# Kernel optimization log

Measured on AMD Instinct MI355X. Metric: run time of the kernel, lower is better.

The kernel has to match this reference:

```python
import jax, jax.numpy as jnp
import numpy as np

DIM = 128
HEADS = 8
HD = DIM // HEADS          # head_dim = 16
KD = HD // 2               # key_dim = 8 (attn_ratio=0.5)
EPS = 1e-3                 # BatchNorm eps
SCALE = KD ** -0.5


def _bn(x, g, b, m, v):
    # eval-mode BatchNorm2d over channel axis (NCHW)
    s = (g / jnp.sqrt(v + EPS))[None, :, None, None]
    return (x - m[None, :, None, None]) * s + b[None, :, None, None]


def _conv1x1(x, w):
    # w: [Cout, Cin, 1, 1]
    return jnp.einsum('oi,bihw->bohw', w[:, :, 0, 0], x)


def _dwconv3(x, w):
    # depthwise 3x3, pad 1; w: [C, 1, 3, 3]
    return jax.lax.conv_general_dilated(
        x, w, window_strides=(1, 1), padding=((1, 1), (1, 1)),
        feature_group_count=x.shape[1],
        dimension_numbers=('NCHW', 'OIHW', 'NCHW'))


def setup_inputs() -> dict:
    key = jax.random.key(0)
    ks = jax.random.split(key, 20)
    H_CH = DIM + 2 * KD * HEADS  # 256
    x = jax.random.normal(ks[0], (4, DIM, 40, 40), dtype=jnp.float32)

    def bn_params(k, c):
        k1, k2, k3, k4 = jax.random.split(k, 4)
        g = 1.0 + 0.1 * jax.random.normal(k1, (c,), jnp.float32)
        b = 0.1 * jax.random.normal(k2, (c,), jnp.float32)
        m = 0.1 * jax.random.normal(k3, (c,), jnp.float32)
        v = jax.random.uniform(k4, (c,), jnp.float32, 0.5, 1.5)
        return g, b, m, v

    qkv_w = 0.05 * jax.random.normal(ks[1], (H_CH, DIM, 1, 1), jnp.float32)
    qkv_g, qkv_b, qkv_m, qkv_v = bn_params(ks[2], H_CH)
    pe_w = 0.05 * jax.random.normal(ks[3], (DIM, 1, 3, 3), jnp.float32)
    pe_g, pe_b, pe_m, pe_v = bn_params(ks[4], DIM)
    proj_w = 0.05 * jax.random.normal(ks[5], (DIM, DIM, 1, 1), jnp.float32)
    proj_g, proj_b, proj_m, proj_v = bn_params(ks[6], DIM)

    return dict(x=x,
                qkv_w=qkv_w, qkv_g=qkv_g, qkv_b=qkv_b, qkv_m=qkv_m, qkv_v=qkv_v,
                pe_w=pe_w, pe_g=pe_g, pe_b=pe_b, pe_m=pe_m, pe_v=pe_v,
                proj_w=proj_w, proj_g=proj_g, proj_b=proj_b, proj_m=proj_m, proj_v=proj_v)


def reference(x, qkv_w, qkv_g, qkv_b, qkv_m, qkv_v,
              pe_w, pe_g, pe_b, pe_m, pe_v,
              proj_w, proj_g, proj_b, proj_m, proj_v):
    b, c, H, W = x.shape
    n = H * W
    qkv = _bn(_conv1x1(x, qkv_w), qkv_g, qkv_b, qkv_m, qkv_v)
    qkv = qkv.reshape(b, HEADS, 2 * KD + HD, n)
    q, k, v = qkv[:, :, :KD], qkv[:, :, KD:2 * KD], qkv[:, :, 2 * KD:]
    # attn[b,h,n,m] = sum_k q[b,h,k,n] * k[b,h,k,m] * scale
    attn = jnp.einsum('bhkn,bhkm->bhnm', q, k) * SCALE
    attn = jax.nn.softmax(attn, axis=-1)
    # out = v @ attn^T : [b,h,hd,n]
    out = jnp.einsum('bhdn,bhmn->bhdm', v, attn).reshape(b, c, H, W)
    pe = _bn(_dwconv3(v.reshape(b, c, H, W), pe_w), pe_g, pe_b, pe_m, pe_v)
    y = _bn(_conv1x1(out + pe, proj_w), proj_g, proj_b, proj_m, proj_v)
    return y
```

## Files before the change

kernel.cpp:

```cpp
#include <hip/hip_runtime.h>
#include <hip/hip_bf16.h>

#define NB 4
#define CDIM 128
#define NPIX 1600
#define WIMG 40
#define HCH 256
#define NHEADS 8
#define KDQ 8
#define HDV 16
#define EPSV 1e-3f
#define SCALEV 0.35355339059327373f
#define KT 320
#define KLP 24
#define VTP (KT + 8)

typedef unsigned short u16;
typedef float f32x4 __attribute__((ext_vector_type(4)));
typedef __bf16 bf16x8 __attribute__((ext_vector_type(8)));

union U16B { uint4 u; bf16x8 v; };

__device__ __forceinline__ u16 f2bf(float f) {
  unsigned u = __float_as_uint(f);
  return (u16)((u + 0x7FFFu + ((u >> 16) & 1u)) >> 16);
}
__device__ __forceinline__ float bf2f(u16 b) {
  return __uint_as_float(((unsigned)b) << 16);
}
__device__ __forceinline__ unsigned cvt_pk_bf16(float lo, float hi) {
  unsigned r;
  asm("v_cvt_pk_bf16_f32 %0, %1, %2" : "=v"(r) : "v"(lo), "v"(hi));
  return r;
}

__global__ __launch_bounds__(512) void k_qkv(
    const float* __restrict__ x, const float* __restrict__ w,
    const float* __restrict__ gg, const float* __restrict__ bb,
    const float* __restrict__ mm, const float* __restrict__ vv,
    float* __restrict__ vf32, u16* __restrict__ qbf,
    u16* __restrict__ kbf, u16* __restrict__ vtbf)
{
  const int pblk = blockIdx.x % 7;
  const int ct   = (blockIdx.x / 7) % (HCH / 8);
  const int b    = blockIdx.x / (7 * (HCH / 8));
  const int tid  = threadIdx.x;
  const int half = tid >> 8;
  const int t    = tid & 255;

  __shared__ float wl[8][CDIM];
  __shared__ float red[256][8];
  for (int i = tid; i < 8 * CDIM; i += 512)
    wl[i >> 7][i & 127] = w[(ct * 8 + (i >> 7)) * CDIM + (i & 127)];
  __syncthreads();

  const int praw = pblk * 256 + t;
  const int p    = praw < NPIX ? praw : NPIX - 1;

  const float* xb = x + (size_t)b * CDIM * NPIX + p;
  float acc[8] = {0.f, 0.f, 0.f, 0.f, 0.f, 0.f, 0.f, 0.f};
  const int c0 = half * 64;
#pragma unroll 4
  for (int ci = c0; ci < c0 + 64; ++ci) {
    const float xv = xb[(size_t)ci * NPIX];
#pragma unroll
    for (int j = 0; j < 8; ++j) acc[j] += wl[j][ci] * xv;
  }

  if (half == 1) {
#pragma unroll
    for (int j = 0; j < 8; ++j) red[t][j] = acc[j];
  }
  __syncthreads();
  if (half == 1 || praw >= NPIX) return;
#pragma unroll
  for (int j = 0; j < 8; ++j) acc[j] += red[t][j];

  const int grp = ct & 3;
  const int h   = ct >> 2;
  float o[8];
#pragma unroll
  for (int j = 0; j < 8; ++j) {
    const int c = ct * 8 + j;
    const float sc = gg[c] * rsqrtf(vv[c] + EPSV);
    const float bi = bb[c] - mm[c] * sc;
    o[j] = acc[j] * sc + bi;
    if (grp == 0) o[j] *= SCALEV;
  }

  if (grp <= 1) {
    u16 hb[8], lb[8];
#pragma unroll
    for (int j = 0; j < 8; ++j) {
      hb[j] = f2bf(o[j]);
      lb[j] = f2bf(o[j] - bf2f(hb[j]));
    }
    uint4 H, L;
    H.x = hb[0] | ((unsigned)hb[1] << 16);
    H.y = hb[2] | ((unsigned)hb[3] << 16);
    H.z = hb[4] | ((unsigned)hb[5] << 16);
    H.w = hb[6] | ((unsigned)hb[7] << 16);
    L.x = lb[0] | ((unsigned)lb[1] << 16);
    L.y = lb[2] | ((unsigned)lb[3] << 16);
    L.z = lb[4] | ((unsigned)lb[5] << 16);
    L.w = lb[6] | ((unsigned)lb[7] << 16);
    u16* dst = (grp == 0) ? qbf : kbf;
    const size_t base = ((size_t)(b * NHEADS + h) * NPIX + p) * 16;
    *(uint4*)&dst[base]     = H;
    *(uint4*)&dst[base + 8] = L;
  } else {
    const int d0 = (grp == 2) ? 0 : 8;
#pragma unroll
    for (int j = 0; j < 8; ++j) {
      vtbf[((size_t)(b * NHEADS + h) * HDV + d0 + j) * NPIX + p] = f2bf(o[j]);
      vf32[((size_t)b * CDIM + h * HDV + d0 + j) * NPIX + p] = o[j];
    }
  }
}

__global__ __launch_bounds__(256) void k_peadd(
    const float* __restrict__ vf32, const float* __restrict__ w,
    const float* __restrict__ gg, const float* __restrict__ bb,
    const float* __restrict__ mm, const float* __restrict__ vv,
    float* __restrict__ atb)
{
  const int idx = blockIdx.x * 256 + threadIdx.x;
  if (idx >= NB * CDIM * NPIX) return;
  const int p  = idx % NPIX;
  const int vc = (idx / NPIX) % CDIM;
  const int yy = p / WIMG, xx = p % WIMG;
  const float* vb = vf32 + (size_t)(idx - p);
  float acc = 0.f;
#pragma unroll
  for (int dy = -1; dy <= 1; ++dy)
#pragma unroll
    for (int dx = -1; dx <= 1; ++dx) {
      const int y2 = yy + dy, x2 = xx + dx;
      if ((unsigned)y2 < (unsigned)WIMG && (unsigned)x2 < (unsigned)WIMG)
        acc += w[vc * 9 + (dy + 1) * 3 + (dx + 1)] * vb[y2 * WIMG + x2];
    }
  const float sc = gg[vc] * rsqrtf(vv[vc] + EPSV);
  const float bi = bb[vc] - mm[vc] * sc;
  atb[idx] += acc * sc + bi;
}

__global__ __launch_bounds__(256) void k_attn(
    const u16* __restrict__ qbf, const u16* __restrict__ kbf,
    const u16* __restrict__ vtbf, float* __restrict__ attno)
{
  const int bh   = blockIdx.x & 31;
  const int qblk = blockIdx.x >> 5;
  const int b = bh >> 3, h = bh & 7;
  const int tid = threadIdx.x;
  const int lane = tid & 63, wid = tid >> 6;
  const int qloc = lane & 15, g = lane >> 4;

  __shared__ __align__(16) u16 Klds[KT][KLP];
  __shared__ __align__(16) u16 Vtlds[HDV][VTP];

  const int qglob = qblk * 64 + wid * 16 + qloc;
  U16B qf;
  qf.u = *(const uint4*)&qbf[((size_t)bh * NPIX + qglob) * 16 + (g & 1) * 8];

  f32x4 c3 = {0.f, 0.f, 0.f, 0.f};
  float lsum = 0.f;
  const int idx0 = (((g & 1) << 5) | qloc) << 2;
  const int idx1 = idx0 + 64;
  const bool selA = (g < 2);
  const f32x4 zf = {0.f, 0.f, 0.f, 0.f};
  const int ksel = (g >> 1) * 8;

  for (int kt = 0; kt < NPIX / KT; ++kt) {
    const int kb0 = kt * KT;
    __syncthreads();
    for (int i = tid; i < KT * 2; i += 256) {
      const int r = i >> 1, hf = (i & 1) * 8;
      *(uint4*)&Klds[r][hf] =
          *(const uint4*)&kbf[((size_t)bh * NPIX + kb0 + r) * 16 + hf];
    }
    for (int c = tid; c < HDV * (KT / 8); c += 256) {
      const int d = c / (KT / 8), n0 = (c % (KT / 8)) * 8;
      *(uint4*)&Vtlds[d][n0] =
          *(const uint4*)&vtbf[((size_t)bh * HDV + d) * NPIX + kb0 + n0];
    }
    __syncthreads();

    for (int ks = 0; ks < KT / 32; ++ks) {
      U16B kfA, kfB;
      kfA.u = *(const uint4*)&Klds[ks * 32 + qloc][ksel];
      kfB.u = *(const uint4*)&Klds[ks * 32 + 16 + qloc][ksel];
      f32x4 cA = __builtin_amdgcn_mfma_f32_16x16x32_bf16(kfA.v, qf.v, zf, 0, 0, 0);
      f32x4 cB = __builtin_amdgcn_mfma_f32_16x16x32_bf16(kfB.v, qf.v, zf, 0, 0, 0);

      const unsigned pkA0 = cvt_pk_bf16(__expf(cA[0]), __expf(cA[1]));
      const unsigned pkA1 = cvt_pk_bf16(__expf(cA[2]), __expf(cA[3]));
      const unsigned pkB0 = cvt_pk_bf16(__expf(cB[0]), __expf(cB[1]));
      const unsigned pkB1 = cvt_pk_bf16(__expf(cB[2]), __expf(cB[3]));

      const int a0 = __builtin_amdgcn_ds_bpermute(idx0, (int)pkA0);
      const int b0 = __builtin_amdgcn_ds_bpermute(idx0, (int)pkB0);
      const int a1 = __builtin_amdgcn_ds_bpermute(idx0, (int)pkA1);
      const int b1 = __builtin_amdgcn_ds_bpermute(idx0, (int)pkB1);
      const int a2 = __builtin_amdgcn_ds_bpermute(idx1, (int)pkA0);
      const int b2 = __builtin_amdgcn_ds_bpermute(idx1, (int)pkB0);
      const int a3 = __builtin_amdgcn_ds_bpermute(idx1, (int)pkA1);
      const int b3 = __builtin_amdgcn_ds_bpermute(idx1, (int)pkB1);
      U16B pf;
      pf.u.x = (unsigned)(selA ? a0 : b0);
      pf.u.y = (unsigned)(selA ? a1 : b1);
      pf.u.z = (unsigned)(selA ? a2 : b2);
      pf.u.w = (unsigned)(selA ? a3 : b3);

      lsum += __uint_as_float(pf.u.x << 16) + __uint_as_float(pf.u.x & 0xFFFF0000u)
            + __uint_as_float(pf.u.y << 16) + __uint_as_float(pf.u.y & 0xFFFF0000u)
            + __uint_as_float(pf.u.z << 16) + __uint_as_float(pf.u.z & 0xFFFF0000u)
            + __uint_as_float(pf.u.w << 16) + __uint_as_float(pf.u.w & 0xFFFF0000u);

      U16B vf4;
      vf4.u = *(const uint4*)&Vtlds[qloc][ks * 32 + g * 8];

      c3 = __builtin_amdgcn_mfma_f32_16x16x32_bf16(vf4.v, pf.v, c3, 0, 0, 0);
    }
  }

  lsum += __shfl_xor(lsum, 16);
  lsum += __shfl_xor(lsum, 32);
  const float rl = 1.f / lsum;

  float* ob = attno + ((size_t)b * CDIM + h * HDV) * NPIX + qblk * 64 + wid * 16 + qloc;
#pragma unroll
  for (int r = 0; r < 4; ++r)
    ob[(size_t)(g * 4 + r) * NPIX] = c3[r] * rl;
}

__global__ __launch_bounds__(256) void k_proj(
    const float* __restrict__ atb, const float* __restrict__ w,
    const float* __restrict__ gg, const float* __restrict__ bb,
    const float* __restrict__ mm, const float* __restrict__ vv,
    float* __restrict__ out)
{
  const int pblk = blockIdx.x % 7;
  const int ct   = (blockIdx.x / 7) % (CDIM / 2);
  const int b    = blockIdx.x / (7 * (CDIM / 2));
  const int tid  = threadIdx.x;

  __shared__ float wl[2][CDIM];
  wl[tid >> 7][tid & 127] = w[(ct * 2 + (tid >> 7)) * CDIM + (tid & 127)];
  __syncthreads();

  const int p = pblk * 256 + tid;
  if (p >= NPIX) return;

  const float* ab = atb + (size_t)b * CDIM * NPIX + p;
  float a0 = 0.f, a1 = 0.f;
#pragma unroll 8
  for (int ci = 0; ci < CDIM; ++ci) {
    const float xv = ab[(size_t)ci * NPIX];
    a0 += wl[0][ci] * xv;
    a1 += wl[1][ci] * xv;
  }
#pragma unroll
  for (int j = 0; j < 2; ++j) {
    const int c = ct * 2 + j;
    const float sc = gg[c] * rsqrtf(vv[c] + EPSV);
    const float bi = bb[c] - mm[c] * sc;
    out[((size_t)b * CDIM + c) * NPIX + p] = (j ? a1 : a0) * sc + bi;
  }
}

extern "C" void kernel_launch(void* const* d_in, const int* in_sizes, int n_in,
                              void* d_out, int out_size, void* d_ws, size_t ws_size,
                              hipStream_t stream)
{
  const float* x      = (const float*)d_in[0];
  const float* qkv_w  = (const float*)d_in[1];
  const float* qkv_g  = (const float*)d_in[2];
  const float* qkv_b  = (const float*)d_in[3];
  const float* qkv_m  = (const float*)d_in[4];
  const float* qkv_v  = (const float*)d_in[5];
  const float* pe_w   = (const float*)d_in[6];
  const float* pe_g   = (const float*)d_in[7];
  const float* pe_b   = (const float*)d_in[8];
  const float* pe_m   = (const float*)d_in[9];
  const float* pe_v   = (const float*)d_in[10];
  const float* proj_w = (const float*)d_in[11];
  const float* proj_g = (const float*)d_in[12];
  const float* proj_b = (const float*)d_in[13];
  const float* proj_m = (const float*)d_in[14];
  const float* proj_v = (const float*)d_in[15];

  float* ws   = (float*)d_ws;
  float* vf32 = ws;
  float* atb  = vf32 + (size_t)NB * CDIM * NPIX;
  u16*   qbf  = (u16*)(atb + (size_t)NB * CDIM * NPIX);
  u16*   kbf  = qbf + (size_t)NB * NHEADS * NPIX * 16;
  u16*   vtbf = kbf + (size_t)NB * NHEADS * NPIX * 16;

  k_qkv<<<dim3(NB * (HCH / 8) * 7), 512, 0, stream>>>(
      x, qkv_w, qkv_g, qkv_b, qkv_m, qkv_v, vf32, qbf, kbf, vtbf);
  k_attn<<<dim3(NB * NHEADS * 25), 256, 0, stream>>>(qbf, kbf, vtbf, atb);
  k_peadd<<<dim3((NB * CDIM * NPIX + 255) / 256), 256, 0, stream>>>(
      vf32, pe_w, pe_g, pe_b, pe_m, pe_v, atb);
  k_proj<<<dim3(NB * (CDIM / 2) * 7), 256, 0, stream>>>(
      atb, proj_w, proj_g, proj_b, proj_m, proj_v, (float*)d_out);
}
```

Before: 153.2 us.

## Fuse depthwise PE conv into attention epilogue and split keys across two wave groups

Removes the separate PE-add kernel by computing the depthwise 3x3 conv plus BatchNorm in the attention kernel's epilogue, writing the final attention-plus-PE sum directly. The attention block grows to 512 threads, and two wave groups each handle half of every key tile. Their partial outputs and row sums are combined through shared memory. This saves a kernel launch and a read-modify-write pass over the intermediate buffer and adds parallelism per block, at the cost of an extra LDS reduction and barrier.

Result: faster. 145.7 us (-4.9%).

```diff
diff --git a/kernel.cpp b/kernel.cpp
--- a/kernel.cpp
+++ b/kernel.cpp
@@ -118,47 +118,26 @@
   }
 }
 
-__global__ __launch_bounds__(256) void k_peadd(
-    const float* __restrict__ vf32, const float* __restrict__ w,
-    const float* __restrict__ gg, const float* __restrict__ bb,
-    const float* __restrict__ mm, const float* __restrict__ vv,
-    float* __restrict__ atb)
-{
-  const int idx = blockIdx.x * 256 + threadIdx.x;
-  if (idx >= NB * CDIM * NPIX) return;
-  const int p  = idx % NPIX;
-  const int vc = (idx / NPIX) % CDIM;
-  const int yy = p / WIMG, xx = p % WIMG;
-  const float* vb = vf32 + (size_t)(idx - p);
-  float acc = 0.f;
-#pragma unroll
-  for (int dy = -1; dy <= 1; ++dy)
-#pragma unroll
-    for (int dx = -1; dx <= 1; ++dx) {
-      const int y2 = yy + dy, x2 = xx + dx;
-      if ((unsigned)y2 < (unsigned)WIMG && (unsigned)x2 < (unsigned)WIMG)
-        acc += w[vc * 9 + (dy + 1) * 3 + (dx + 1)] * vb[y2 * WIMG + x2];
-    }
-  const float sc = gg[vc] * rsqrtf(vv[vc] + EPSV);
-  const float bi = bb[vc] - mm[vc] * sc;
-  atb[idx] += acc * sc + bi;
-}
-
-__global__ __launch_bounds__(256) void k_attn(
+__global__ __launch_bounds__(512) void k_attn(
     const u16* __restrict__ qbf, const u16* __restrict__ kbf,
-    const u16* __restrict__ vtbf, float* __restrict__ attno)
+    const u16* __restrict__ vtbf, const float* __restrict__ vf32,
+    const float* __restrict__ pw, const float* __restrict__ pg,
+    const float* __restrict__ pbb, const float* __restrict__ pm,
+    const float* __restrict__ pv, float* __restrict__ atb)
 {
   const int bh   = blockIdx.x & 31;
   const int qblk = blockIdx.x >> 5;
   const int b = bh >> 3, h = bh & 7;
   const int tid = threadIdx.x;
   const int lane = tid & 63, wid = tid >> 6;
+  const int qw = wid & 3, kh = wid >> 2;
   const int qloc = lane & 15, g = lane >> 4;
 
   __shared__ __align__(16) u16 Klds[KT][KLP];
   __shared__ __align__(16) u16 Vtlds[HDV][VTP];
-
-  const int qglob = qblk * 64 + wid * 16 + qloc;
+  __shared__ float red[256][6];
+
+  const int qglob = qblk * 64 + qw * 16 + qloc;
   U16B qf;
   qf.u = *(const uint4*)&qbf[((size_t)bh * NPIX + qglob) * 16 + (g & 1) * 8];
 
@@ -173,19 +152,19 @@
   for (int kt = 0; kt < NPIX / KT; ++kt) {
     const int kb0 = kt * KT;
     __syncthreads();
-    for (int i = tid; i < KT * 2; i += 256) {
+    for (int i = tid; i < KT * 2; i += 512) {
       const int r = i >> 1, hf = (i & 1) * 8;
       *(uint4*)&Klds[r][hf] =
           *(const uint4*)&kbf[((size_t)bh * NPIX + kb0 + r) * 16 + hf];
     }
-    for (int c = tid; c < HDV * (KT / 8); c += 256) {
+    for (int c = tid; c < HDV * (KT / 8); c += 512) {
       const int d = c / (KT / 8), n0 = (c % (KT / 8)) * 8;
       *(uint4*)&Vtlds[d][n0] =
           *(const uint4*)&vtbf[((size_t)bh * HDV + d) * NPIX + kb0 + n0];
     }
     __syncthreads();
 
-    for (int ks = 0; ks < KT / 32; ++ks) {
+    for (int ks = kh * 5; ks < kh * 5 + 5; ++ks) {
       U16B kfA, kfB;
       kfA.u = *(const uint4*)&Klds[ks * 32 + qloc][ksel];
       kfB.u = *(const uint4*)&Klds[ks * 32 + 16 + qloc][ksel];
@@ -223,14 +202,46 @@
     }
   }
 
+  if (kh == 1) {
+    const int rr = qw * 64 + lane;
+    red[rr][0] = c3[0]; red[rr][1] = c3[1];
+    red[rr][2] = c3[2]; red[rr][3] = c3[3];
+    red[rr][4] = lsum;
+  }
+  __syncthreads();
+  if (kh == 1) return;
+  {
+    const int rr = qw * 64 + lane;
+    c3[0] += red[rr][0]; c3[1] += red[rr][1];
+    c3[2] += red[rr][2]; c3[3] += red[rr][3];
+    lsum  += red[rr][4];
+  }
+
   lsum += __shfl_xor(lsum, 16);
   lsum += __shfl_xor(lsum, 32);
   const float rl = 1.f / lsum;
 
-  float* ob = attno + ((size_t)b * CDIM + h * HDV) * NPIX + qblk * 64 + wid * 16 + qloc;
-#pragma unroll
-  for (int r = 0; r < 4; ++r)
-    ob[(size_t)(g * 4 + r) * NPIX] = c3[r] * rl;
+  const int p  = qblk * 64 + qw * 16 + qloc;
+  const int yy = p / WIMG, xx = p % WIMG;
+  const float* vb = vf32 + ((size_t)b * CDIM + h * HDV) * NPIX;
+  float* ob = atb + ((size_t)b * CDIM + h * HDV) * NPIX + p;
+#pragma unroll
+  for (int r = 0; r < 4; ++r) {
+    const int d = g * 4 + r;
+    const int c = h * HDV + d;
+    float acc = 0.f;
+#pragma unroll
+    for (int dy = -1; dy <= 1; ++dy)
+#pragma unroll
+      for (int dx = -1; dx <= 1; ++dx) {
+        const int y2 = yy + dy, x2 = xx + dx;
+        if ((unsigned)y2 < (unsigned)WIMG && (unsigned)x2 < (unsigned)WIMG)
+          acc += pw[c * 9 + (dy + 1) * 3 + (dx + 1)] * vb[(size_t)d * NPIX + y2 * WIMG + x2];
+      }
+    const float sc = pg[c] * rsqrtf(pv[c] + EPSV);
+    const float bi = pbb[c] - pm[c] * sc;
+    ob[(size_t)d * NPIX] = c3[r] * rl + acc * sc + bi;
+  }
 }
 
 __global__ __launch_bounds__(256) void k_proj(
@@ -298,9 +309,8 @@
 
   k_qkv<<<dim3(NB * (HCH / 8) * 7), 512, 0, stream>>>(
       x, qkv_w, qkv_g, qkv_b, qkv_m, qkv_v, vf32, qbf, kbf, vtbf);
-  k_attn<<<dim3(NB * NHEADS * 25), 256, 0, stream>>>(qbf, kbf, vtbf, atb);
-  k_peadd<<<dim3((NB * CDIM * NPIX + 255) / 256), 256, 0, stream>>>(
-      vf32, pe_w, pe_g, pe_b, pe_m, pe_v, atb);
+  k_attn<<<dim3(NB * NHEADS * 25), 512, 0, stream>>>(
+      qbf, kbf, vtbf, vf32, pe_w, pe_g, pe_b, pe_m, pe_v, atb);
   k_proj<<<dim3(NB * (CDIM / 2) * 7), 256, 0, stream>>>(
       atb, proj_w, proj_g, proj_b, proj_m, proj_v, (float*)d_out);
 }
```
